# Kernel tuning notes

Measured on AMD Instinct MI355X. Metric: run time of the kernel, lower is better.

The kernel has to match this reference:

```python
import jax, jax.numpy as jnp
import numpy as np

H = 256
L = 5
B = 1024
NL, EL = 65536, 262144
NP_, EP = 131072, 524288
BN_EPS = 1e-5


def _bn_relu(x, gamma, beta):
    # BatchNorm1d (training mode, biased variance) followed by ReLU
    m = x.mean(axis=0)
    v = ((x - m) ** 2).mean(axis=0)
    return jax.nn.relu((x - m) * jax.lax.rsqrt(v + BN_EPS) * gamma + beta)


def _gin_conv(h, src, dst, W1, b1, W2, b2):
    # GINConv, eps=0: mlp(x + sum_{j->i} x_j)
    agg = jax.ops.segment_sum(h[src], dst, num_segments=h.shape[0])
    z = h + agg
    return jax.nn.relu(z @ W1 + b1) @ W2 + b2


def _forward(lig_x, prot_x, lig_embed_W, lig_embed_b, prot_embed_W, prot_embed_b,
             lig_virtual0, prot_virtual0,
             lig_conv_W1, lig_conv_b1, lig_conv_W2, lig_conv_b2,
             lig_vmlp_W, lig_vmlp_b, lig_vmlp_gamma, lig_vmlp_beta,
             prot_conv_W1, prot_conv_b1, prot_conv_W2, prot_conv_b2,
             prot_vmlp_W, prot_vmlp_b, prot_vmlp_gamma, prot_vmlp_beta,
             pred_W1, pred_b1, pred_W2, pred_b2,
             lig_batch, prot_batch, lig_edge_index, prot_edge_index):
    lig_h = lig_x @ lig_embed_W + lig_embed_b        # [NL, H]
    prot_h = prot_x @ prot_embed_W + prot_embed_b    # [NP, H]
    lig_v = jnp.broadcast_to(lig_virtual0, (B, H))
    prot_v = jnp.broadcast_to(prot_virtual0, (B, H))
    l_src, l_dst = lig_edge_index[0], lig_edge_index[1]
    p_src, p_dst = prot_edge_index[0], prot_edge_index[1]
    for i in range(L):
        # ligand branch: virtual-node pool -> MLP -> broadcast, then GIN conv (residual)
        lig_v = lig_v + jax.ops.segment_sum(lig_h, lig_batch, num_segments=B)
        lig_v = _bn_relu(lig_v @ lig_vmlp_W[i] + lig_vmlp_b[i], lig_vmlp_gamma[i], lig_vmlp_beta[i])
        lig_h = lig_h + lig_v[lig_batch]
        lig_h = lig_h + _gin_conv(lig_h, l_src, l_dst, lig_conv_W1[i], lig_conv_b1[i], lig_conv_W2[i], lig_conv_b2[i])
        # protein branch
        prot_v = prot_v + jax.ops.segment_sum(prot_h, prot_batch, num_segments=B)
        prot_v = _bn_relu(prot_v @ prot_vmlp_W[i] + prot_vmlp_b[i], prot_vmlp_gamma[i], prot_vmlp_beta[i])
        prot_h = prot_h + prot_v[prot_batch]
        prot_h = prot_h + _gin_conv(prot_h, p_src, p_dst, prot_conv_W1[i], prot_conv_b1[i], prot_conv_W2[i], prot_conv_b2[i])
    lig_cnt = jax.ops.segment_sum(jnp.ones((lig_h.shape[0],), lig_h.dtype), lig_batch, num_segments=B)
    prot_cnt = jax.ops.segment_sum(jnp.ones((prot_h.shape[0],), prot_h.dtype), prot_batch, num_segments=B)
    lig_pool = jax.ops.segment_sum(lig_h, lig_batch, num_segments=B) / lig_cnt[:, None]
    prot_pool = jax.ops.segment_sum(prot_h, prot_batch, num_segments=B) / prot_cnt[:, None]
    combined = jnp.concatenate([lig_pool, prot_pool], axis=-1)  # [B, 2H]
    return jax.nn.relu(combined @ pred_W1 + pred_b1) @ pred_W2 + pred_b2  # [B, 1]


def setup_inputs() -> dict:
    key = jax.random.key(0)
    ks = jax.random.split(key, 40)
    s = 0.05
    inp = {
        'lig_x': jax.random.normal(ks[0], (NL, 26), jnp.float32),
        'prot_x': jax.random.normal(ks[1], (NP_, 20), jnp.float32),
        'lig_embed_W': jax.random.normal(ks[2], (26, H), jnp.float32) * s,
        'lig_embed_b': jnp.zeros((H,), jnp.float32),
        'prot_embed_W': jax.random.normal(ks[3], (20, H), jnp.float32) * s,
        'prot_embed_b': jnp.zeros((H,), jnp.float32),
        'lig_virtual0': jax.random.normal(ks[4], (1, H), jnp.float32),
        'prot_virtual0': jax.random.normal(ks[5], (1, H), jnp.float32),
        'lig_conv_W1': jax.random.normal(ks[6], (L, H, H), jnp.float32) * s,
        'lig_conv_b1': jnp.zeros((L, H), jnp.float32),
        'lig_conv_W2': jax.random.normal(ks[7], (L, H, H), jnp.float32) * s,
        'lig_conv_b2': jnp.zeros((L, H), jnp.float32),
        'lig_vmlp_W': jax.random.normal(ks[8], (L, H, H), jnp.float32) * s,
        'lig_vmlp_b': jnp.zeros((L, H), jnp.float32),
        'lig_vmlp_gamma': jnp.ones((L, H), jnp.float32),
        'lig_vmlp_beta': jnp.zeros((L, H), jnp.float32),
        'prot_conv_W1': jax.random.normal(ks[9], (L, H, H), jnp.float32) * s,
        'prot_conv_b1': jnp.zeros((L, H), jnp.float32),
        'prot_conv_W2': jax.random.normal(ks[10], (L, H, H), jnp.float32) * s,
        'prot_conv_b2': jnp.zeros((L, H), jnp.float32),
        'prot_vmlp_W': jax.random.normal(ks[11], (L, H, H), jnp.float32) * s,
        'prot_vmlp_b': jnp.zeros((L, H), jnp.float32),
        'prot_vmlp_gamma': jnp.ones((L, H), jnp.float32),
        'prot_vmlp_beta': jnp.zeros((L, H), jnp.float32),
        'pred_W1': jax.random.normal(ks[12], (2 * H, H), jnp.float32) * s,
        'pred_b1': jnp.zeros((H,), jnp.float32),
        'pred_W2': jax.random.normal(ks[13], (H, 1), jnp.float32) * s,
        'pred_b2': jnp.zeros((1,), jnp.float32),
        # sorted batch ids covering all B graphs (PyG-style contiguous batching)
        'lig_batch': (jnp.arange(NL, dtype=jnp.int32) * B) // NL,
        'prot_batch': (jnp.arange(NP_, dtype=jnp.int32) * B) // NP_,
        'lig_edge_index': jax.random.randint(ks[14], (2, EL), 0, NL, jnp.int32),
        'prot_edge_index': jax.random.randint(ks[15], (2, EP), 0, NP_, jnp.int32),
    }
    return inp


def reference(lig_x, prot_x, lig_embed_W, lig_embed_b, prot_embed_W, prot_embed_b,
              lig_virtual0, prot_virtual0,
              lig_conv_W1, lig_conv_b1, lig_conv_W2, lig_conv_b2,
              lig_vmlp_W, lig_vmlp_b, lig_vmlp_gamma, lig_vmlp_beta,
              prot_conv_W1, prot_conv_b1, prot_conv_W2, prot_conv_b2,
              prot_vmlp_W, prot_vmlp_b, prot_vmlp_gamma, prot_vmlp_beta,
              pred_W1, pred_b1, pred_W2, pred_b2,
              lig_batch, prot_batch, lig_edge_index, prot_edge_index):
    return _forward(lig_x, prot_x, lig_embed_W, lig_embed_b, prot_embed_W, prot_embed_b,
                    lig_virtual0, prot_virtual0,
                    lig_conv_W1, lig_conv_b1, lig_conv_W2, lig_conv_b2,
                    lig_vmlp_W, lig_vmlp_b, lig_vmlp_gamma, lig_vmlp_beta,
                    prot_conv_W1, prot_conv_b1, prot_conv_W2, prot_conv_b2,
                    prot_vmlp_W, prot_vmlp_b, prot_vmlp_gamma, prot_vmlp_beta,
                    pred_W1, pred_b1, pred_W2, pred_b2,
                    lig_batch, prot_batch, lig_edge_index, prot_edge_index)
```

## Files before the change

kernel.cpp:

```cpp
#include <hip/hip_runtime.h>

#define H_DIM 256
#define NLAYER 5
#define BGRAPH 1024
#define CAP 24

typedef __attribute__((ext_vector_type(8))) short short8;
typedef __attribute__((ext_vector_type(4))) float f32x4;
typedef const __attribute__((address_space(1))) unsigned int* gas_ptr;
typedef __attribute__((address_space(3))) unsigned int* las_ptr;

struct __align__(8) us4 { unsigned short x, y, z, w; };

__device__ __forceinline__ float b2f(unsigned short u) {
    union { float f; unsigned v; } c; c.v = ((unsigned)u) << 16; return c.f;
}
__device__ __forceinline__ unsigned short f2b(float f) {
    union { float f; unsigned v; } c; c.f = f;
    return (unsigned short)((c.v + 0x7fffu + ((c.v >> 16) & 1u)) >> 16);
}

__global__ __launch_bounds__(256) void embed_kernel(
    const float* __restrict__ x, const float* __restrict__ W,
    const float* __restrict__ b, unsigned short* __restrict__ h, int K)
{
    __shared__ float xs[256];
    const int m0 = blockIdx.x * 8;
    const int tid = threadIdx.x;
    if (tid < 8 * K) xs[tid] = x[(size_t)m0 * K + tid];
    __syncthreads();
    const int n = tid;
    float acc[8] = {0.f,0.f,0.f,0.f,0.f,0.f,0.f,0.f};
    for (int k = 0; k < K; ++k) {
        const float w = W[k * H_DIM + n];
        #pragma unroll
        for (int r = 0; r < 8; ++r) acc[r] += xs[r * K + k] * w;
    }
    const float bb = b[n];
    #pragma unroll
    for (int r = 0; r < 8; ++r)
        h[(size_t)(m0 + r) * H_DIM + n] = f2b(acc[r] + bb);
}

__global__ __launch_bounds__(256) void init_v_kernel(
    const float* __restrict__ lig0, const float* __restrict__ prot0,
    float* __restrict__ lig_v, float* __restrict__ prot_v)
{
    const int b = blockIdx.x, n = threadIdx.x;
    lig_v[b * H_DIM + n]  = lig0[n];
    prot_v[b * H_DIM + n] = prot0[n];
}

__global__ __launch_bounds__(256) void wprep_kernel(
    const float* __restrict__ W, unsigned short* __restrict__ Wt)
{
    __shared__ float t[64][65];
    const int l = blockIdx.z;
    const int k0 = blockIdx.x * 64, n0 = blockIdx.y * 64;
    const int tid = threadIdx.x;
    const int c = tid & 63, r4 = tid >> 6;
    const float* Wl = W + (size_t)l * 65536;
    unsigned short* Wtl = Wt + (size_t)l * 65536;
    #pragma unroll
    for (int i = 0; i < 16; ++i) {
        const int r = i * 4 + r4;
        t[r][c] = Wl[(size_t)(k0 + r) * 256 + n0 + c];
    }
    __syncthreads();
    #pragma unroll
    for (int i = 0; i < 16; ++i) {
        const int nn = i * 4 + r4;
        const int n = n0 + nn;
        const int x = (n >> 1) & 3;
        const int s = ((c >> 3) & 3) ^ x;
        const int kaddr = k0 + (c & ~31) + (s << 3) + (c & 7);
        Wtl[(size_t)n * 256 + kaddr] = f2b(t[c][nn]);
    }
}

__global__ __launch_bounds__(256) void bucket_build_kernel(
    const int* __restrict__ src, const int* __restrict__ dst, int E,
    int* __restrict__ deg, int* __restrict__ bucket)
{
    const int e = blockIdx.x * 256 + threadIdx.x;
    if (e >= E) return;
    const int d = dst[e], s = src[e];
    const int slot = atomicAdd(&deg[d], 1);
    if (slot < CAP) bucket[(size_t)d * CAP + slot] = s;
}

__global__ __launch_bounds__(256) void pool_add_kernel(
    const unsigned short* __restrict__ h, float* __restrict__ v, int cnt)
{
    const int b = blockIdx.x, n = threadIdx.x;
    const unsigned short* hp = &h[(size_t)b * cnt * H_DIM + n];
    float s = 0.f;
    #pragma unroll 8
    for (int r = 0; r < cnt; ++r) s += b2f(hp[(size_t)r * H_DIM]);
    v[b * H_DIM + n] += s;
}

__global__ __launch_bounds__(256) void v_add_kernel(
    float* __restrict__ v, const float* __restrict__ hsum)
{
    const int idx = blockIdx.x * 256 + threadIdx.x;
    v[idx] += hsum[idx];
}

template<bool RELU>
__global__ __launch_bounds__(256) void gemm_small_kernel(
    const float* __restrict__ A, const float* __restrict__ W,
    const float* __restrict__ bias, float* __restrict__ C,
    int M, int N, int K)
{
    constexpr int BM = 32, BN = 64, BK = 32, TM = 2;
    __shared__ __align__(16) float As[BK][BM + 4];
    __shared__ __align__(16) float Bs[BK][BN];
    const int tid = threadIdx.x;
    const int tx = tid & 15;
    const int ty = tid >> 4;
    const int m0 = blockIdx.x * BM;
    const int n0 = blockIdx.y * BN;

    float acc[TM][4] = {};

    for (int kt = 0; kt < K; kt += BK) {
        {
            const int row = tid >> 3, kq = tid & 7;
            const float4 a = *(const float4*)&A[(size_t)(m0 + row) * K + kt + kq * 4];
            As[kq * 4 + 0][row] = a.x;
            As[kq * 4 + 1][row] = a.y;
            As[kq * 4 + 2][row] = a.z;
            As[kq * 4 + 3][row] = a.w;
        }
        #pragma unroll
        for (int i = 0; i < 2; ++i) {
            const int f = tid + i * 256;
            const int row = f >> 4, c4 = f & 15;
            *(float4*)&Bs[row][c4 * 4] =
                *(const float4*)&W[(size_t)(kt + row) * N + n0 + c4 * 4];
        }
        __syncthreads();
        #pragma unroll
        for (int kk = 0; kk < BK; ++kk) {
            const float4 bv = *(const float4*)&Bs[kk][tx * 4];
            #pragma unroll
            for (int im = 0; im < TM; ++im) {
                const float a = As[kk][ty * TM + im];
                acc[im][0] += a * bv.x; acc[im][1] += a * bv.y;
                acc[im][2] += a * bv.z; acc[im][3] += a * bv.w;
            }
        }
        __syncthreads();
    }

    const float4 bb = *(const float4*)&bias[n0 + tx * 4];
    #pragma unroll
    for (int im = 0; im < TM; ++im) {
        const int m = m0 + ty * TM + im;
        float4 r;
        r.x = acc[im][0] + bb.x; r.y = acc[im][1] + bb.y;
        r.z = acc[im][2] + bb.z; r.w = acc[im][3] + bb.w;
        if constexpr (RELU) {
            r.x = fmaxf(r.x, 0.f); r.y = fmaxf(r.y, 0.f);
            r.z = fmaxf(r.z, 0.f); r.w = fmaxf(r.w, 0.f);
        }
        *(float4*)&C[(size_t)m * N + n0 + tx * 4] = r;
    }
}

__global__ __launch_bounds__(512) void conv_fused2_kernel(
    const unsigned short* __restrict__ Hin,
    const int* __restrict__ deg, const int* __restrict__ bucket,
    const int* __restrict__ batch, const float* __restrict__ v,
    const unsigned short* __restrict__ Wt1, const float* __restrict__ b1,
    const unsigned short* __restrict__ Wt2, const float* __restrict__ b2,
    unsigned short* __restrict__ Hout, float* __restrict__ hsum)
{
    constexpr int K = 256, BK = 32;
    __shared__ __align__(16) unsigned short U[64 * 264];
    __shared__ __align__(16) unsigned short Bs[256 * 32];
    const int tid  = threadIdx.x;
    const int lane = tid & 63;
    const int wid  = tid >> 6;
    const int wr   = wid >> 2;
    const int wc   = wid & 3;
    const int q    = lane >> 4;
    const int l15  = lane & 15;
    const int m0   = blockIdx.x * 64;
    const int albase = (tid & ~63) * 16;
    const int bq0  = batch[m0];
    const float* __restrict__ vg = v + (size_t)bq0 * H_DIM;

    {
        const float4 vm = *(const float4*)&vg[lane * 4];
        for (int r8 = 0; r8 < 8; ++r8) {
            const int lr = wid * 8 + r8;
            const int m = m0 + lr;
            const us4 hv = *(const us4*)&Hin[(size_t)m * H_DIM + lane * 4];
            float4 acc = { b2f(hv.x) + vm.x, b2f(hv.y) + vm.y,
                           b2f(hv.z) + vm.z, b2f(hv.w) + vm.w };
            int cnt = deg[m]; if (cnt > CAP) cnt = CAP;
            const int* bp = &bucket[(size_t)m * CAP];
            for (int i = 0; i < cnt; i += 4) {
                const int4 s4 = *(const int4*)&bp[i];
                const int rem = cnt - i;
                us4 a0, a1, a2, a3;
                int q0, q1, q2, q3;
                a0 = *(const us4*)&Hin[(size_t)s4.x * H_DIM + lane * 4];
                q0 = batch[s4.x];
                if (rem > 1) { a1 = *(const us4*)&Hin[(size_t)s4.y * H_DIM + lane * 4]; q1 = batch[s4.y]; }
                if (rem > 2) { a2 = *(const us4*)&Hin[(size_t)s4.z * H_DIM + lane * 4]; q2 = batch[s4.z]; }
                if (rem > 3) { a3 = *(const us4*)&Hin[(size_t)s4.w * H_DIM + lane * 4]; q3 = batch[s4.w]; }
                {
                    const float4 w0 = *(const float4*)&v[(size_t)q0 * H_DIM + lane * 4];
                    acc.x += b2f(a0.x) + w0.x; acc.y += b2f(a0.y) + w0.y;
                    acc.z += b2f(a0.z) + w0.z; acc.w += b2f(a0.w) + w0.w;
                }
                if (rem > 1) {
                    const float4 w1 = *(const float4*)&v[(size_t)q1 * H_DIM + lane * 4];
                    acc.x += b2f(a1.x) + w1.x; acc.y += b2f(a1.y) + w1.y;
                    acc.z += b2f(a1.z) + w1.z; acc.w += b2f(a1.w) + w1.w;
                }
                if (rem > 2) {
                    const float4 w2 = *(const float4*)&v[(size_t)q2 * H_DIM + lane * 4];
                    acc.x += b2f(a2.x) + w2.x; acc.y += b2f(a2.y) + w2.y;
                    acc.z += b2f(a2.z) + w2.z; acc.w += b2f(a2.w) + w2.w;
                }
                if (rem > 3) {
                    const float4 w3 = *(const float4*)&v[(size_t)q3 * H_DIM + lane * 4];
                    acc.x += b2f(a3.x) + w3.x; acc.y += b2f(a3.y) + w3.y;
                    acc.z += b2f(a3.z) + w3.z; acc.w += b2f(a3.w) + w3.w;
                }
            }
            us4 o = { f2b(acc.x), f2b(acc.y), f2b(acc.z), f2b(acc.w) };
            const int ab = lr * 512 + ((lane * 8) ^ ((lr & 7) << 4));
            *(us4*)((char*)U + ab) = o;
        }
    }
    __syncthreads();

    f32x4 acc[2][4];
    #pragma unroll
    for (int i = 0; i < 2; ++i)
        #pragma unroll
        for (int j = 0; j < 4; ++j) acc[i][j] = (f32x4){0.f, 0.f, 0.f, 0.f};

    for (int kt = 0; kt < K; kt += BK) {
        #pragma unroll
        for (int i = 0; i < 2; ++i) {
            const int c = tid + i * 512;
            __builtin_amdgcn_global_load_lds(
                (gas_ptr)&Wt1[(size_t)(c >> 2) * K + kt + (c & 3) * 8],
                (las_ptr)((char*)Bs + albase + i * 8192), 16, 0, 0);
        }
        __syncthreads();
        short8 av[2], bv[4];
        #pragma unroll
        for (int mi = 0; mi < 2; ++mi) {
            const int lrow = wr * 32 + mi * 16 + l15;
            const int ab = lrow * 512 + ((kt * 2 + q * 16) ^ ((lrow & 7) << 4));
            av[mi] = *(const short8*)((char*)U + ab);
        }
        #pragma unroll
        for (int ni = 0; ni < 4; ++ni) {
            const int n = wc * 64 + ni * 16 + l15;
            const int bb = n * 64 + ((q * 16) ^ (((n >> 1) & 3) << 4));
            bv[ni] = *(const short8*)((char*)Bs + bb);
        }
        #pragma unroll
        for (int mi = 0; mi < 2; ++mi)
            #pragma unroll
            for (int ni = 0; ni < 4; ++ni)
                acc[mi][ni] = __builtin_amdgcn_mfma_f32_16x16x32_bf16(
                    av[mi], bv[ni], acc[mi][ni], 0, 0, 0);
        __syncthreads();
    }

    #pragma unroll
    for (int ni = 0; ni < 4; ++ni) {
        const int col = wc * 64 + ni * 16 + l15;
        const float bb = b1[col];
        #pragma unroll
        for (int mi = 0; mi < 2; ++mi)
            #pragma unroll
            for (int j = 0; j < 4; ++j) {
                const int row = wr * 32 + mi * 16 + q * 4 + j;
                U[row * 264 + col] = f2b(fmaxf(acc[mi][ni][j] + bb, 0.f));
            }
    }
    #pragma unroll
    for (int i = 0; i < 2; ++i)
        #pragma unroll
        for (int j = 0; j < 4; ++j) acc[i][j] = (f32x4){0.f, 0.f, 0.f, 0.f};
    __syncthreads();

    for (int kt = 0; kt < K; kt += BK) {
        #pragma unroll
        for (int i = 0; i < 2; ++i) {
            const int c = tid + i * 512;
            __builtin_amdgcn_global_load_lds(
                (gas_ptr)&Wt2[(size_t)(c >> 2) * K + kt + (c & 3) * 8],
                (las_ptr)((char*)Bs + albase + i * 8192), 16, 0, 0);
        }
        __syncthreads();
        short8 av[2], bv[4];
        #pragma unroll
        for (int mi = 0; mi < 2; ++mi) {
            const int lrow = wr * 32 + mi * 16 + l15;
            av[mi] = *(const short8*)&U[lrow * 264 + kt + q * 8];
        }
        #pragma unroll
        for (int ni = 0; ni < 4; ++ni) {
            const int n = wc * 64 + ni * 16 + l15;
            const int bb = n * 64 + ((q * 16) ^ (((n >> 1) & 3) << 4));
            bv[ni] = *(const short8*)((char*)Bs + bb);
        }
        #pragma unroll
        for (int mi = 0; mi < 2; ++mi)
            #pragma unroll
            for (int ni = 0; ni < 4; ++ni)
                acc[mi][ni] = __builtin_amdgcn_mfma_f32_16x16x32_bf16(
                    av[mi], bv[ni], acc[mi][ni], 0, 0, 0);
        __syncthreads();
    }

    float* hl = (float*)Bs;
    if (tid < 256) hl[tid] = 0.f;
    __syncthreads();

    int cols[4]; float b2c[4], vc[4];
    #pragma unroll
    for (int ni = 0; ni < 4; ++ni) {
        cols[ni] = wc * 64 + ni * 16 + l15;
        b2c[ni] = b2[cols[ni]];
        vc[ni]  = vg[cols[ni]];
    }
    float lsum[4] = {0.f, 0.f, 0.f, 0.f};
    #pragma unroll
    for (int mi = 0; mi < 2; ++mi)
        #pragma unroll
        for (int j = 0; j < 4; ++j) {
            const int row = m0 + wr * 32 + mi * 16 + q * 4 + j;
            const unsigned short* hip_ = &Hin[(size_t)row * H_DIM];
            unsigned short* hop = &Hout[(size_t)row * H_DIM];
            #pragma unroll
            for (int ni = 0; ni < 4; ++ni) {
                const float val = b2f(hip_[cols[ni]]) + vc[ni]
                                + acc[mi][ni][j] + b2c[ni];
                hop[cols[ni]] = f2b(val);
                lsum[ni] += val;
            }
        }
    #pragma unroll
    for (int ni = 0; ni < 4; ++ni) atomicAdd(&hl[cols[ni]], lsum[ni]);
    __syncthreads();
    if (tid < 256) atomicAdd(&hsum[(size_t)bq0 * H_DIM + tid], hl[tid]);
}

__global__ __launch_bounds__(256) void bn_part_kernel(
    const float* __restrict__ vtmp, float* __restrict__ part)
{
    const int g = blockIdx.x, n = threadIdx.x;
    float s = 0.f, s2 = 0.f;
    #pragma unroll 8
    for (int r = 0; r < 32; ++r) {
        const float x = vtmp[(size_t)(g * 32 + r) * H_DIM + n];
        s += x; s2 += x * x;
    }
    part[g * H_DIM + n] = s;
    part[32 * H_DIM + g * H_DIM + n] = s2;
}

__global__ __launch_bounds__(256) void bn_finalize_kernel(
    const float* __restrict__ part, const float* __restrict__ gamma,
    const float* __restrict__ beta, float* __restrict__ scale,
    float* __restrict__ shift)
{
    const int n = threadIdx.x;
    float s = 0.f, s2 = 0.f;
    #pragma unroll 8
    for (int g = 0; g < 32; ++g) {
        s  += part[g * H_DIM + n];
        s2 += part[32 * H_DIM + g * H_DIM + n];
    }
    const float mean = s * (1.f / BGRAPH);
    const float var  = s2 * (1.f / BGRAPH) - mean * mean;
    const float sc   = gamma[n] * rsqrtf(var + 1e-5f);
    scale[n] = sc;
    shift[n] = beta[n] - mean * sc;
}

__global__ __launch_bounds__(256) void bn_relu_kernel(
    const float* __restrict__ vtmp, const float* __restrict__ scale,
    const float* __restrict__ shift, float* __restrict__ v)
{
    const int idx = blockIdx.x * 256 + threadIdx.x;
    const int n = idx & 255;
    v[idx] = fmaxf(vtmp[idx] * scale[n] + shift[n], 0.f);
}

__global__ __launch_bounds__(256) void pool_hsum_kernel(
    const float* __restrict__ hl, const float* __restrict__ hp,
    float* __restrict__ comb)
{
    const int b = blockIdx.x, n = threadIdx.x;
    comb[(size_t)b * 512 + n]       = hl[(size_t)b * H_DIM + n] * (1.f / 64.f);
    comb[(size_t)b * 512 + 256 + n] = hp[(size_t)b * H_DIM + n] * (1.f / 128.f);
}

__global__ __launch_bounds__(256) void pred_final_kernel(
    const float* __restrict__ hidden, const float* __restrict__ W2,
    const float* __restrict__ b2, float* __restrict__ out)
{
    const int b = blockIdx.x, t = threadIdx.x;
    float p = hidden[(size_t)b * H_DIM + t] * W2[t];
    #pragma unroll
    for (int off = 32; off >= 1; off >>= 1) p += __shfl_down(p, off);
    __shared__ float red[4];
    if ((t & 63) == 0) red[t >> 6] = p;
    __syncthreads();
    if (t == 0) out[b] = red[0] + red[1] + red[2] + red[3] + b2[0];
}

extern "C" void kernel_launch(void* const* d_in, const int* in_sizes, int n_in,
                              void* d_out, int out_size, void* d_ws, size_t ws_size,
                              hipStream_t stream)
{
    const int NL = 65536, NP = 131072, EL = 262144, EP = 524288;
    const int B = BGRAPH, H = H_DIM;

    const float* lig_x        = (const float*)d_in[0];
    const float* prot_x       = (const float*)d_in[1];
    const float* lig_embed_W  = (const float*)d_in[2];
    const float* lig_embed_b  = (const float*)d_in[3];
    const float* prot_embed_W = (const float*)d_in[4];
    const float* prot_embed_b = (const float*)d_in[5];
    const float* lig_virtual0 = (const float*)d_in[6];
    const float* prot_virtual0= (const float*)d_in[7];
    const float* lig_conv_W1  = (const float*)d_in[8];
    const float* lig_conv_b1  = (const float*)d_in[9];
    const float* lig_conv_W2  = (const float*)d_in[10];
    const float* lig_conv_b2  = (const float*)d_in[11];
    const float* lig_vmlp_W   = (const float*)d_in[12];
    const float* lig_vmlp_b   = (const float*)d_in[13];
    const float* lig_vmlp_g   = (const float*)d_in[14];
    const float* lig_vmlp_be  = (const float*)d_in[15];
    const float* prot_conv_W1 = (const float*)d_in[16];
    const float* prot_conv_b1 = (const float*)d_in[17];
    const float* prot_conv_W2 = (const float*)d_in[18];
    const float* prot_conv_b2 = (const float*)d_in[19];
    const float* prot_vmlp_W  = (const float*)d_in[20];
    const float* prot_vmlp_b  = (const float*)d_in[21];
    const float* prot_vmlp_g  = (const float*)d_in[22];
    const float* prot_vmlp_be = (const float*)d_in[23];
    const float* pred_W1      = (const float*)d_in[24];
    const float* pred_b1      = (const float*)d_in[25];
    const float* pred_W2      = (const float*)d_in[26];
    const float* pred_b2      = (const float*)d_in[27];
    const int* lig_batch      = (const int*)d_in[28];
    const int* prot_batch     = (const int*)d_in[29];
    const int* lig_ei         = (const int*)d_in[30];
    const int* prot_ei        = (const int*)d_in[31];

    float* ws = (float*)d_ws;
    float* lig_v    = ws;
    float* prot_v   = lig_v    + (size_t)B * H;
    float* vtmp     = prot_v   + (size_t)B * H;
    float* scale    = vtmp     + (size_t)B * H;
    float* shift    = scale    + H;
    float* part     = shift    + H;
    float* comb     = part     + 64 * H;
    float* hidden   = comb     + (size_t)B * 2 * H;
    float* hsum_lig = hidden   + (size_t)B * H;
    float* hsum_prot= hsum_lig + (size_t)B * H;
    unsigned short* lig_h0  = (unsigned short*)(hsum_prot + (size_t)B * H);
    unsigned short* lig_h1  = lig_h0  + (size_t)NL * H;
    unsigned short* prot_h0 = lig_h1  + (size_t)NL * H;
    unsigned short* prot_h1 = prot_h0 + (size_t)NP * H;
    unsigned short* wt_lw1  = prot_h1 + (size_t)NP * H;
    unsigned short* wt_lw2  = wt_lw1 + (size_t)NLAYER * H * H;
    unsigned short* wt_pw1  = wt_lw2 + (size_t)NLAYER * H * H;
    unsigned short* wt_pw2  = wt_pw1 + (size_t)NLAYER * H * H;
    int* deg_lig  = (int*)(wt_pw2 + (size_t)NLAYER * H * H);
    int* deg_prot = deg_lig  + NL;
    int* bkt_lig  = deg_prot + NP;
    int* bkt_prot = bkt_lig  + (size_t)NL * CAP;

    hipMemsetAsync(deg_lig, 0, (size_t)(NL + NP) * sizeof(int), stream);
    bucket_build_kernel<<<EL / 256, 256, 0, stream>>>(
        lig_ei, lig_ei + EL, EL, deg_lig, bkt_lig);
    bucket_build_kernel<<<EP / 256, 256, 0, stream>>>(
        prot_ei, prot_ei + EP, EP, deg_prot, bkt_prot);
    wprep_kernel<<<dim3(4, 4, NLAYER), 256, 0, stream>>>(lig_conv_W1, wt_lw1);
    wprep_kernel<<<dim3(4, 4, NLAYER), 256, 0, stream>>>(lig_conv_W2, wt_lw2);
    wprep_kernel<<<dim3(4, 4, NLAYER), 256, 0, stream>>>(prot_conv_W1, wt_pw1);
    wprep_kernel<<<dim3(4, 4, NLAYER), 256, 0, stream>>>(prot_conv_W2, wt_pw2);

    embed_kernel<<<NL / 8, 256, 0, stream>>>(lig_x, lig_embed_W, lig_embed_b, lig_h0, 26);
    embed_kernel<<<NP / 8, 256, 0, stream>>>(prot_x, prot_embed_W, prot_embed_b, prot_h0, 20);
    init_v_kernel<<<B, 256, 0, stream>>>(lig_virtual0, prot_virtual0, lig_v, prot_v);

    auto layer = [&](int i, unsigned short* h_in, unsigned short* h_out,
                     int Nn, int cnt, float* v, float* hsum,
                     const float* vW, const float* vb, const float* vg, const float* vbe,
                     const unsigned short* Wt1, const float* b1,
                     const unsigned short* Wt2, const float* b2,
                     const int* batch, const int* deg, const int* bkt) {
        if (i == 0)
            pool_add_kernel<<<B, 256, 0, stream>>>(h_in, v, cnt);
        else
            v_add_kernel<<<B, 256, 0, stream>>>(v, hsum);
        gemm_small_kernel<false><<<dim3(B / 32, 4), 256, 0, stream>>>(
            v, vW, vb, vtmp, B, H, H);
        bn_part_kernel<<<32, 256, 0, stream>>>(vtmp, part);
        bn_finalize_kernel<<<1, 256, 0, stream>>>(part, vg, vbe, scale, shift);
        bn_relu_kernel<<<B, 256, 0, stream>>>(vtmp, scale, shift, v);
        hipMemsetAsync(hsum, 0, (size_t)B * H * sizeof(float), stream);
        conv_fused2_kernel<<<Nn / 64, 512, 0, stream>>>(
            h_in, deg, bkt, batch, v, Wt1, b1, Wt2, b2, h_out, hsum);
    };

    for (int i = 0; i < NLAYER; ++i) {
        const size_t wo = (size_t)i * H * H;
        const size_t bo = (size_t)i * H;
        unsigned short* lin  = (i & 1) ? lig_h1  : lig_h0;
        unsigned short* lout = (i & 1) ? lig_h0  : lig_h1;
        unsigned short* pin  = (i & 1) ? prot_h1 : prot_h0;
        unsigned short* pout = (i & 1) ? prot_h0 : prot_h1;
        layer(i, lin, lout, NL, 64, lig_v, hsum_lig,
              lig_vmlp_W + wo, lig_vmlp_b + bo, lig_vmlp_g + bo, lig_vmlp_be + bo,
              wt_lw1 + wo, lig_conv_b1 + bo, wt_lw2 + wo, lig_conv_b2 + bo,
              lig_batch, deg_lig, bkt_lig);
        layer(i, pin, pout, NP, 128, prot_v, hsum_prot,
              prot_vmlp_W + wo, prot_vmlp_b + bo, prot_vmlp_g + bo, prot_vmlp_be + bo,
              wt_pw1 + wo, prot_conv_b1 + bo, wt_pw2 + wo, prot_conv_b2 + bo,
              prot_batch, deg_prot, bkt_prot);
    }

    pool_hsum_kernel<<<B, 256, 0, stream>>>(hsum_lig, hsum_prot, comb);
    gemm_small_kernel<true><<<dim3(B / 32, 4), 256, 0, stream>>>(
        comb, pred_W1, pred_b1, hidden, B, H, 2 * H);
    pred_final_kernel<<<B, 256, 0, stream>>>(hidden, pred_W2, pred_b2, (float*)d_out);
}
```

Before: 1.849 ms.

## Batch lig/prot virtual-node MLP, fuse BN stats, and load MFMA weights pre-fragmented

Merges the ligand and protein virtual-node MLP steps into single launches. The GEMM folds in the hsum add and accumulates the BatchNorm sum and sum-of-squares with atomics, and a single apply kernel then normalises both branches. This replaces the v_add, bn_part, bn_finalize and bn_relu launches. The conv kernel now reads weights straight from global memory in a pre-shuffled MFMA fragment layout instead of staging them through LDS with a barrier per k-step, so it needs less shared memory. The risks are more global weight traffic per block, which relies on cache hits, and variance computed from atomically accumulated E[x^2]-mean^2.

```diff
diff --git a/kernel.cpp b/kernel.cpp
--- a/kernel.cpp
+++ b/kernel.cpp
@@ -7,8 +7,6 @@
 
 typedef __attribute__((ext_vector_type(8))) short short8;
 typedef __attribute__((ext_vector_type(4))) float f32x4;
-typedef const __attribute__((address_space(1))) unsigned int* gas_ptr;
-typedef __attribute__((address_space(3))) unsigned int* las_ptr;
 
 struct __align__(8) us4 { unsigned short x, y, z, w; };
 
@@ -51,31 +49,27 @@
     prot_v[b * H_DIM + n] = prot0[n];
 }
 
-__global__ __launch_bounds__(256) void wprep_kernel(
-    const float* __restrict__ W, unsigned short* __restrict__ Wt)
-{
-    __shared__ float t[64][65];
-    const int l = blockIdx.z;
-    const int k0 = blockIdx.x * 64, n0 = blockIdx.y * 64;
-    const int tid = threadIdx.x;
-    const int c = tid & 63, r4 = tid >> 6;
+__global__ __launch_bounds__(64) void wprep_kernel(
+    const float* __restrict__ W, unsigned short* __restrict__ Wf)
+{
+    const int kb = blockIdx.x, nb = blockIdx.y, l = blockIdx.z;
+    const int lane = threadIdx.x, q = lane >> 4, l15 = lane & 15;
     const float* Wl = W + (size_t)l * 65536;
-    unsigned short* Wtl = Wt + (size_t)l * 65536;
-    #pragma unroll
-    for (int i = 0; i < 16; ++i) {
-        const int r = i * 4 + r4;
-        t[r][c] = Wl[(size_t)(k0 + r) * 256 + n0 + c];
-    }
-    __syncthreads();
-    #pragma unroll
-    for (int i = 0; i < 16; ++i) {
-        const int nn = i * 4 + r4;
-        const int n = n0 + nn;
-        const int x = (n >> 1) & 3;
-        const int s = ((c >> 3) & 3) ^ x;
-        const int kaddr = k0 + (c & ~31) + (s << 3) + (c & 7);
-        Wtl[(size_t)n * 256 + kaddr] = f2b(t[c][nn]);
-    }
+    unsigned short* dst = Wf + (size_t)l * 65536
+                        + ((size_t)(kb * 16 + nb) * 64 + lane) * 8;
+    const int kbase = kb * 32 + q * 8;
+    const int n = nb * 16 + l15;
+    us4 o0, o1;
+    o0.x = f2b(Wl[(size_t)(kbase + 0) * 256 + n]);
+    o0.y = f2b(Wl[(size_t)(kbase + 1) * 256 + n]);
+    o0.z = f2b(Wl[(size_t)(kbase + 2) * 256 + n]);
+    o0.w = f2b(Wl[(size_t)(kbase + 3) * 256 + n]);
+    o1.x = f2b(Wl[(size_t)(kbase + 4) * 256 + n]);
+    o1.y = f2b(Wl[(size_t)(kbase + 5) * 256 + n]);
+    o1.z = f2b(Wl[(size_t)(kbase + 6) * 256 + n]);
+    o1.w = f2b(Wl[(size_t)(kbase + 7) * 256 + n]);
+    *(us4*)dst = o0;
+    *(us4*)(dst + 4) = o1;
 }
 
 __global__ __launch_bounds__(256) void bucket_build_kernel(
@@ -89,33 +83,40 @@
     if (slot < CAP) bucket[(size_t)d * CAP + slot] = s;
 }
 
-__global__ __launch_bounds__(256) void pool_add_kernel(
-    const unsigned short* __restrict__ h, float* __restrict__ v, int cnt)
-{
-    const int b = blockIdx.x, n = threadIdx.x;
+__global__ __launch_bounds__(256) void pool0_kernel(
+    const unsigned short* __restrict__ hL, const unsigned short* __restrict__ hP,
+    float* __restrict__ hsL, float* __restrict__ hsP)
+{
+    const int br = blockIdx.y, b = blockIdx.x, n = threadIdx.x;
+    const unsigned short* h = br ? hP : hL;
+    float* hs = br ? hsP : hsL;
+    const int cnt = br ? 128 : 64;
     const unsigned short* hp = &h[(size_t)b * cnt * H_DIM + n];
     float s = 0.f;
     #pragma unroll 8
     for (int r = 0; r < cnt; ++r) s += b2f(hp[(size_t)r * H_DIM]);
-    v[b * H_DIM + n] += s;
-}
-
-__global__ __launch_bounds__(256) void v_add_kernel(
-    float* __restrict__ v, const float* __restrict__ hsum)
-{
-    const int idx = blockIdx.x * 256 + threadIdx.x;
-    v[idx] += hsum[idx];
-}
-
-template<bool RELU>
-__global__ __launch_bounds__(256) void gemm_small_kernel(
-    const float* __restrict__ A, const float* __restrict__ W,
-    const float* __restrict__ bias, float* __restrict__ C,
-    int M, int N, int K)
-{
-    constexpr int BM = 32, BN = 64, BK = 32, TM = 2;
+    hs[(size_t)b * H_DIM + n] = s;
+}
+
+__global__ __launch_bounds__(256) void vmlp_gemm_kernel(
+    const float* __restrict__ vL, const float* __restrict__ hsL,
+    const float* __restrict__ WL, const float* __restrict__ bL,
+    const float* __restrict__ vP, const float* __restrict__ hsP,
+    const float* __restrict__ WP, const float* __restrict__ bP,
+    float* __restrict__ vtL, float* __restrict__ vtP,
+    float* __restrict__ part)
+{
+    constexpr int BM = 32, BN = 64, BK = 32, TM = 2, K = H_DIM, N = H_DIM;
     __shared__ __align__(16) float As[BK][BM + 4];
     __shared__ __align__(16) float Bs[BK][BN];
+    __shared__ float st[2][64];
+    const int br = blockIdx.z;
+    const float* v    = br ? vP  : vL;
+    const float* hsum = br ? hsP : hsL;
+    const float* W    = br ? WP  : WL;
+    const float* bias = br ? bP  : bL;
+    float* vt = br ? vtP : vtL;
+    float* pt = part + br * 512;
     const int tid = threadIdx.x;
     const int tx = tid & 15;
     const int ty = tid >> 4;
@@ -127,7 +128,10 @@
     for (int kt = 0; kt < K; kt += BK) {
         {
             const int row = tid >> 3, kq = tid & 7;
-            const float4 a = *(const float4*)&A[(size_t)(m0 + row) * K + kt + kq * 4];
+            const size_t ao = (size_t)(m0 + row) * K + kt + kq * 4;
+            float4 a = *(const float4*)&v[ao];
+            const float4 h4 = *(const float4*)&hsum[ao];
+            a.x += h4.x; a.y += h4.y; a.z += h4.z; a.w += h4.w;
             As[kq * 4 + 0][row] = a.x;
             As[kq * 4 + 1][row] = a.y;
             As[kq * 4 + 2][row] = a.z;
@@ -154,32 +158,72 @@
         __syncthreads();
     }
 
+    if (tid < 128) ((float*)st)[tid] = 0.f;
+    __syncthreads();
+
     const float4 bb = *(const float4*)&bias[n0 + tx * 4];
+    float cs[4] = {0.f,0.f,0.f,0.f}, cq[4] = {0.f,0.f,0.f,0.f};
     #pragma unroll
     for (int im = 0; im < TM; ++im) {
         const int m = m0 + ty * TM + im;
         float4 r;
         r.x = acc[im][0] + bb.x; r.y = acc[im][1] + bb.y;
         r.z = acc[im][2] + bb.z; r.w = acc[im][3] + bb.w;
-        if constexpr (RELU) {
-            r.x = fmaxf(r.x, 0.f); r.y = fmaxf(r.y, 0.f);
-            r.z = fmaxf(r.z, 0.f); r.w = fmaxf(r.w, 0.f);
-        }
-        *(float4*)&C[(size_t)m * N + n0 + tx * 4] = r;
-    }
-}
-
-__global__ __launch_bounds__(512) void conv_fused2_kernel(
+        *(float4*)&vt[(size_t)m * N + n0 + tx * 4] = r;
+        cs[0] += r.x; cq[0] += r.x * r.x;
+        cs[1] += r.y; cq[1] += r.y * r.y;
+        cs[2] += r.z; cq[2] += r.z * r.z;
+        cs[3] += r.w; cq[3] += r.w * r.w;
+    }
+    #pragma unroll
+    for (int c = 0; c < 4; ++c) {
+        atomicAdd(&st[0][tx * 4 + c], cs[c]);
+        atomicAdd(&st[1][tx * 4 + c], cq[c]);
+    }
+    __syncthreads();
+    if (tid < 64) {
+        atomicAdd(&pt[n0 + tid], st[0][tid]);
+        atomicAdd(&pt[256 + n0 + tid], st[1][tid]);
+    }
+}
+
+__global__ __launch_bounds__(256) void vmlp_apply_kernel(
+    const float* __restrict__ part,
+    const float* __restrict__ gL, const float* __restrict__ beL,
+    const float* __restrict__ gP, const float* __restrict__ beP,
+    const float* __restrict__ vtL, const float* __restrict__ vtP,
+    float* __restrict__ vL, float* __restrict__ vP)
+{
+    const int br = blockIdx.y, n = threadIdx.x;
+    const float* pt = part + br * 512;
+    const float* g  = br ? gP  : gL;
+    const float* be = br ? beP : beL;
+    const float* vt = br ? vtP : vtL;
+    float* v = br ? vP : vL;
+    const float s  = pt[n];
+    const float s2 = pt[256 + n];
+    const float mean = s * (1.f / BGRAPH);
+    const float var  = s2 * (1.f / BGRAPH) - mean * mean;
+    const float sc = g[n] * rsqrtf(var + 1e-5f);
+    const float sh = be[n] - mean * sc;
+    #pragma unroll
+    for (int r = 0; r < 4; ++r) {
+        const size_t i = (size_t)(blockIdx.x * 4 + r) * H_DIM + n;
+        v[i] = fmaxf(vt[i] * sc + sh, 0.f);
+    }
+}
+
+__global__ __launch_bounds__(512) void conv_fused3_kernel(
     const unsigned short* __restrict__ Hin,
     const int* __restrict__ deg, const int* __restrict__ bucket,
     const int* __restrict__ batch, const float* __restrict__ v,
-    const unsigned short* __restrict__ Wt1, const float* __restrict__ b1,
-    const unsigned short* __restrict__ Wt2, const float* __restrict__ b2,
+    const unsigned short* __restrict__ Wf1, const float* __restrict__ b1,
+    const unsigned short* __restrict__ Wf2, const float* __restrict__ b2,
     unsigned short* __restrict__ Hout, float* __restrict__ hsum)
 {
-    constexpr int K = 256, BK = 32;
-    __shared__ __align__(16) unsigned short U[64 * 264];
-    __shared__ __align__(16) unsigned short Bs[256 * 32];
+    __shared__ __align__(16) unsigned short U[64 * 256];
+    __shared__ float hl[256];
+    char* Ub = (char*)U;
     const int tid  = threadIdx.x;
     const int lane = tid & 63;
     const int wid  = tid >> 6;
@@ -188,9 +232,10 @@
     const int q    = lane >> 4;
     const int l15  = lane & 15;
     const int m0   = blockIdx.x * 64;
-    const int albase = (tid & ~63) * 16;
     const int bq0  = batch[m0];
     const float* __restrict__ vg = v + (size_t)bq0 * H_DIM;
+
+    if (tid < 256) hl[tid] = 0.f;
 
     {
         const float4 vm = *(const float4*)&vg[lane * 4];
@@ -235,7 +280,7 @@
             }
             us4 o = { f2b(acc.x), f2b(acc.y), f2b(acc.z), f2b(acc.w) };
             const int ab = lr * 512 + ((lane * 8) ^ ((lr & 7) << 4));
-            *(us4*)((char*)U + ab) = o;
+            *(us4*)(Ub + ab) = o;
         }
     }
     __syncthreads();
@@ -246,36 +291,26 @@
         #pragma unroll
         for (int j = 0; j < 4; ++j) acc[i][j] = (f32x4){0.f, 0.f, 0.f, 0.f};
 
-    for (int kt = 0; kt < K; kt += BK) {
-        #pragma unroll
-        for (int i = 0; i < 2; ++i) {
-            const int c = tid + i * 512;
-            __builtin_amdgcn_global_load_lds(
-                (gas_ptr)&Wt1[(size_t)(c >> 2) * K + kt + (c & 3) * 8],
-                (las_ptr)((char*)Bs + albase + i * 8192), 16, 0, 0);
-        }
-        __syncthreads();
-        short8 av[2], bv[4];
-        #pragma unroll
-        for (int mi = 0; mi < 2; ++mi) {
-            const int lrow = wr * 32 + mi * 16 + l15;
-            const int ab = lrow * 512 + ((kt * 2 + q * 16) ^ ((lrow & 7) << 4));
-            av[mi] = *(const short8*)((char*)U + ab);
-        }
+    const int arow = wr * 32 + l15;
+    const int rowb0 = arow * 512;
+    const int rowb1 = rowb0 + 16 * 512;
+    const int xorv = (l15 & 7) << 4;
+    const unsigned short* wb1 = Wf1 + ((size_t)(wc * 4) * 64 + lane) * 8;
+    const unsigned short* wb2 = Wf2 + ((size_t)(wc * 4) * 64 + lane) * 8;
+
+    #pragma unroll 2
+    for (int kb = 0; kb < 8; ++kb) {
+        const int c0 = (kb * 64 + q * 16) ^ xorv;
+        const short8 av0 = *(const short8*)(Ub + rowb0 + c0);
+        const short8 av1 = *(const short8*)(Ub + rowb1 + c0);
         #pragma unroll
         for (int ni = 0; ni < 4; ++ni) {
-            const int n = wc * 64 + ni * 16 + l15;
-            const int bb = n * 64 + ((q * 16) ^ (((n >> 1) & 3) << 4));
-            bv[ni] = *(const short8*)((char*)Bs + bb);
-        }
-        #pragma unroll
-        for (int mi = 0; mi < 2; ++mi)
-            #pragma unroll
-            for (int ni = 0; ni < 4; ++ni)
-                acc[mi][ni] = __builtin_amdgcn_mfma_f32_16x16x32_bf16(
-                    av[mi], bv[ni], acc[mi][ni], 0, 0, 0);
-        __syncthreads();
-    }
+            const short8 bv = *(const short8*)&wb1[(size_t)kb * 8192 + ni * 512];
+            acc[0][ni] = __builtin_amdgcn_mfma_f32_16x16x32_bf16(av0, bv, acc[0][ni], 0, 0, 0);
+            acc[1][ni] = __builtin_amdgcn_mfma_f32_16x16x32_bf16(av1, bv, acc[1][ni], 0, 0, 0);
+        }
+    }
+    __syncthreads();
 
     #pragma unroll
     for (int ni = 0; ni < 4; ++ni) {
@@ -286,7 +321,8 @@
             #pragma unroll
             for (int j = 0; j < 4; ++j) {
                 const int row = wr * 32 + mi * 16 + q * 4 + j;
-                U[row * 264 + col] = f2b(fmaxf(acc[mi][ni][j] + bb, 0.f));
+                const int tb = row * 512 + ((col * 2) ^ ((row & 7) << 4));
+                *(unsigned short*)(Ub + tb) = f2b(fmaxf(acc[mi][ni][j] + bb, 0.f));
             }
     }
     #pragma unroll
@@ -295,39 +331,18 @@
         for (int j = 0; j < 4; ++j) acc[i][j] = (f32x4){0.f, 0.f, 0.f, 0.f};
     __syncthreads();
 
-    for (int kt = 0; kt < K; kt += BK) {
-        #pragma unroll
-        for (int i = 0; i < 2; ++i) {
-            const int c = tid + i * 512;
-            __builtin_amdgcn_global_load_lds(
-                (gas_ptr)&Wt2[(size_t)(c >> 2) * K + kt + (c & 3) * 8],
-                (las_ptr)((char*)Bs + albase + i * 8192), 16, 0, 0);
-        }
-        __syncthreads();
-        short8 av[2], bv[4];
-        #pragma unroll
-        for (int mi = 0; mi < 2; ++mi) {
-            const int lrow = wr * 32 + mi * 16 + l15;
-            av[mi] = *(const short8*)&U[lrow * 264 + kt + q * 8];
-        }
+    #pragma unroll 2
+    for (int kb = 0; kb < 8; ++kb) {
+        const int c0 = (kb * 64 + q * 16) ^ xorv;
+        const short8 av0 = *(const short8*)(Ub + rowb0 + c0);
+        const short8 av1 = *(const short8*)(Ub + rowb1 + c0);
         #pragma unroll
         for (int ni = 0; ni < 4; ++ni) {
-            const int n = wc * 64 + ni * 16 + l15;
-            const int bb = n * 64 + ((q * 16) ^ (((n >> 1) & 3) << 4));
-            bv[ni] = *(const short8*)((char*)Bs + bb);
-        }
-        #pragma unroll
-        for (int mi = 0; mi < 2; ++mi)
-            #pragma unroll
-            for (int ni = 0; ni < 4; ++ni)
-                acc[mi][ni] = __builtin_amdgcn_mfma_f32_16x16x32_bf16(
-                    av[mi], bv[ni], acc[mi][ni], 0, 0, 0);
-        __syncthreads();
-    }
-
-    float* hl = (float*)Bs;
-    if (tid < 256) hl[tid] = 0.f;
-    __syncthreads();
+            const short8 bv = *(const short8*)&wb2[(size_t)kb * 8192 + ni * 512];
+            acc[0][ni] = __builtin_amdgcn_mfma_f32_16x16x32_bf16(av0, bv, acc[0][ni], 0, 0, 0);
+            acc[1][ni] = __builtin_amdgcn_mfma_f32_16x16x32_bf16(av1, bv, acc[1][ni], 0, 0, 0);
+        }
+    }
 
     int cols[4]; float b2c[4], vc[4];
     #pragma unroll
@@ -358,46 +373,66 @@
     if (tid < 256) atomicAdd(&hsum[(size_t)bq0 * H_DIM + tid], hl[tid]);
 }
 
-__global__ __launch_bounds__(256) void bn_part_kernel(
-    const float* __restrict__ vtmp, float* __restrict__ part)
-{
-    const int g = blockIdx.x, n = threadIdx.x;
-    float s = 0.f, s2 = 0.f;
-    #pragma unroll 8
-    for (int r = 0; r < 32; ++r) {
-        const float x = vtmp[(size_t)(g * 32 + r) * H_DIM + n];
-        s += x; s2 += x * x;
-    }
-    part[g * H_DIM + n] = s;
-    part[32 * H_DIM + g * H_DIM + n] = s2;
-}
-
-__global__ __launch_bounds__(256) void bn_finalize_kernel(
-    const float* __restrict__ part, const float* __restrict__ gamma,
-    const float* __restrict__ beta, float* __restrict__ scale,
-    float* __restrict__ shift)
-{
-    const int n = threadIdx.x;
-    float s = 0.f, s2 = 0.f;
-    #pragma unroll 8
-    for (int g = 0; g < 32; ++g) {
-        s  += part[g * H_DIM + n];
-        s2 += part[32 * H_DIM + g * H_DIM + n];
-    }
-    const float mean = s * (1.f / BGRAPH);
-    const float var  = s2 * (1.f / BGRAPH) - mean * mean;
-    const float sc   = gamma[n] * rsqrtf(var + 1e-5f);
-    scale[n] = sc;
-    shift[n] = beta[n] - mean * sc;
-}
-
-__global__ __launch_bounds__(256) void bn_relu_kernel(
-    const float* __restrict__ vtmp, const float* __restrict__ scale,
-    const float* __restrict__ shift, float* __restrict__ v)
-{
-    const int idx = blockIdx.x * 256 + threadIdx.x;
-    const int n = idx & 255;
-    v[idx] = fmaxf(vtmp[idx] * scale[n] + shift[n], 0.f);
+template<bool RELU>
+__global__ __launch_bounds__(256) void gemm_small_kernel(
+    const float* __restrict__ A, const float* __restrict__ W,
+    const float* __restrict__ bias, float* __restrict__ C,
+    int M, int N, int K)
+{
+    constexpr int BM = 32, BN = 64, BK = 32, TM = 2;
+    __shared__ __align__(16) float As[BK][BM + 4];
+    __shared__ __align__(16) float Bs[BK][BN];
+    const int tid = threadIdx.x;
+    const int tx = tid & 15;
+    const int ty = tid >> 4;
+    const int m0 = blockIdx.x * BM;
+    const int n0 = blockIdx.y * BN;
+
+    float acc[TM][4] = {};
+
+    for (int kt = 0; kt < K; kt += BK) {
+        {
+            const int row = tid >> 3, kq = tid & 7;
+            const float4 a = *(const float4*)&A[(size_t)(m0 + row) * K + kt + kq * 4];
+            As[kq * 4 + 0][row] = a.x;
+            As[kq * 4 + 1][row] = a.y;
+            As[kq * 4 + 2][row] = a.z;
+            As[kq * 4 + 3][row] = a.w;
+        }
+        #pragma unroll
+        for (int i = 0; i < 2; ++i) {
+            const int f = tid + i * 256;
+            const int row = f >> 4, c4 = f & 15;
+            *(float4*)&Bs[row][c4 * 4] =
+                *(const float4*)&W[(size_t)(kt + row) * N + n0 + c4 * 4];
+        }
+        __syncthreads();
+        #pragma unroll
+        for (int kk = 0; kk < BK; ++kk) {
+            const float4 bv = *(const float4*)&Bs[kk][tx * 4];
+            #pragma unroll
+            for (int im = 0; im < TM; ++im) {
+                const float a = As[kk][ty * TM + im];
+                acc[im][0] += a * bv.x; acc[im][1] += a * bv.y;
+                acc[im][2] += a * bv.z; acc[im][3] += a * bv.w;
+            }
+        }
+        __syncthreads();
+    }
+
+    const float4 bb = *(const float4*)&bias[n0 + tx * 4];
+    #pragma unroll
+    for (int im = 0; im < TM; ++im) {
+        const int m = m0 + ty * TM + im;
+        float4 r;
+        r.x = acc[im][0] + bb.x; r.y = acc[im][1] + bb.y;
+        r.z = acc[im][2] + bb.z; r.w = acc[im][3] + bb.w;
+        if constexpr (RELU) {
+            r.x = fmaxf(r.x, 0.f); r.y = fmaxf(r.y, 0.f);
+            r.z = fmaxf(r.z, 0.f); r.w = fmaxf(r.w, 0.f);
+        }
+        *(float4*)&C[(size_t)m * N + n0 + tx * 4] = r;
+    }
 }
 
 __global__ __launch_bounds__(256) void pool_hsum_kernel(
@@ -466,11 +501,10 @@
     float* ws = (float*)d_ws;
     float* lig_v    = ws;
     float* prot_v   = lig_v    + (size_t)B * H;
-    float* vtmp     = prot_v   + (size_t)B * H;
-    float* scale    = vtmp     + (size_t)B * H;
-    float* shift    = scale    + H;
-    float* part     = shift    + H;
-    float* comb     = part     + 64 * H;
+    float* vtmpL    = prot_v   + (size_t)B * H;
+    float* vtmpP    = vtmpL    + (size_t)B * H;
+    float* part     = vtmpP    + (size_t)B * H;
+    float* comb     = part     + 1024;
     float* hidden   = comb     + (size_t)B * 2 * H;
     float* hsum_lig = hidden   + (size_t)B * H;
     float* hsum_prot= hsum_lig + (size_t)B * H;
@@ -478,11 +512,11 @@
     unsigned short* lig_h1  = lig_h0  + (size_t)NL * H;
     unsigned short* prot_h0 = lig_h1  + (size_t)NL * H;
     unsigned short* prot_h1 = prot_h0 + (size_t)NP * H;
-    unsigned short* wt_lw1  = prot_h1 + (size_t)NP * H;
-    unsigned short* wt_lw2  = wt_lw1 + (size_t)NLAYER * H * H;
-    unsigned short* wt_pw1  = wt_lw2 + (size_t)NLAYER * H * H;
-    unsigned short* wt_pw2  = wt_pw1 + (size_t)NLAYER * H * H;
-    int* deg_lig  = (int*)(wt_pw2 + (size_t)NLAYER * H * H);
+    unsigned short* wf_lw1  = prot_h1 + (size_t)NP * H;
+    unsigned short* wf_lw2  = wf_lw1 + (size_t)NLAYER * H * H;
+    unsigned short* wf_pw1  = wf_lw2 + (size_t)NLAYER * H * H;
+    unsigned short* wf_pw2  = wf_pw1 + (size_t)NLAYER * H * H;
+    int* deg_lig  = (int*)(wf_pw2 + (size_t)NLAYER * H * H);
     int* deg_prot = deg_lig  + NL;
     int* bkt_lig  = deg_prot + NP;
     int* bkt_prot = bkt_lig  + (size_t)NL * CAP;
@@ -492,34 +526,15 @@
         lig_ei, lig_ei + EL, EL, deg_lig, bkt_lig);
     bucket_build_kernel<<<EP / 256, 256, 0, stream>>>(
         prot_ei, prot_ei + EP, EP, deg_prot, bkt_prot);
-    wprep_kernel<<<dim3(4, 4, NLAYER), 256, 0, stream>>>(lig_conv_W1, wt_lw1);
-    wprep_kernel<<<dim3(4, 4, NLAYER), 256, 0, stream>>>(lig_conv_W2, wt_lw2);
-    wprep_kernel<<<dim3(4, 4, NLAYER), 256, 0, stream>>>(prot_conv_W1, wt_pw1);
-    wprep_kernel<<<dim3(4, 4, NLAYER), 256, 0, stream>>>(prot_conv_W2, wt_pw2);
+    wprep_kernel<<<dim3(8, 16, NLAYER), 64, 0, stream>>>(lig_conv_W1, wf_lw1);
+    wprep_kernel<<<dim3(8, 16, NLAYER), 64, 0, stream>>>(lig_conv_W2, wf_lw2);
+    wprep_kernel<<<dim3(8, 16, NLAYER), 64, 0, stream>>>(prot_conv_W1, wf_pw1);
+    wprep_kernel<<<dim3(8, 16, NLAYER), 64, 0, stream>>>(prot_conv_W2, wf_pw2);
 
     embed_kernel<<<NL / 8, 256, 0, stream>>>(lig_x, lig_embed_W, lig_embed_b, lig_h0, 26);
     embed_kernel<<<NP / 8, 256, 0, stream>>>(prot_x, prot_embed_W, prot_embed_b, prot_h0, 20);
     init_v_kernel<<<B, 256, 0, stream>>>(lig_virtual0, prot_virtual0, lig_v, prot_v);
-
-    auto layer = [&](int i, unsigned short* h_in, unsigned short* h_out,
-                     int Nn, int cnt, float* v, float* hsum,
-                     const float* vW, const float* vb, const float* vg, const float* vbe,
-                     const unsigned short* Wt1, const float* b1,
-                     const unsigned short* Wt2, const float* b2,
-                     const int* batch, const int* deg, const int* bkt) {
-        if (i == 0)
-            pool_add_kernel<<<B, 256, 0, stream>>>(h_in, v, cnt);
-        else
-            v_add_kernel<<<B, 256, 0, stream>>>(v, hsum);
-        gemm_small_kernel<false><<<dim3(B / 32, 4), 256, 0, stream>>>(
-            v, vW, vb, vtmp, B, H, H);
-        bn_part_kernel<<<32, 256, 0, stream>>>(vtmp, part);
-        bn_finalize_kernel<<<1, 256, 0, stream>>>(part, vg, vbe, scale, shift);
-        bn_relu_kernel<<<B, 256, 0, stream>>>(vtmp, scale, shift, v);
-        hipMemsetAsync(hsum, 0, (size_t)B * H * sizeof(float), stream);
-        conv_fused2_kernel<<<Nn / 64, 512, 0, stream>>>(
-            h_in, deg, bkt, batch, v, Wt1, b1, Wt2, b2, h_out, hsum);
-    };
+    pool0_kernel<<<dim3(B, 2), 256, 0, stream>>>(lig_h0, prot_h0, hsum_lig, hsum_prot);
 
     for (int i = 0; i < NLAYER; ++i) {
         const size_t wo = (size_t)i * H * H;
@@ -528,14 +543,25 @@
         unsigned short* lout = (i & 1) ? lig_h0  : lig_h1;
         unsigned short* pin  = (i & 1) ? prot_h1 : prot_h0;
         unsigned short* pout = (i & 1) ? prot_h0 : prot_h1;
-        layer(i, lin, lout, NL, 64, lig_v, hsum_lig,
-              lig_vmlp_W + wo, lig_vmlp_b + bo, lig_vmlp_g + bo, lig_vmlp_be + bo,
-              wt_lw1 + wo, lig_conv_b1 + bo, wt_lw2 + wo, lig_conv_b2 + bo,
-              lig_batch, deg_lig, bkt_lig);
-        layer(i, pin, pout, NP, 128, prot_v, hsum_prot,
-              prot_vmlp_W + wo, prot_vmlp_b + bo, prot_vmlp_g + bo, prot_vmlp_be + bo,
-              wt_pw1 + wo, prot_conv_b1 + bo, wt_pw2 + wo, prot_conv_b2 + bo,
-              prot_batch, deg_prot, bkt_prot);
+
+        hipMemsetAsync(part, 0, 1024 * sizeof(float), stream);
+        vmlp_gemm_kernel<<<dim3(32, 4, 2), 256, 0, stream>>>(
+            lig_v, hsum_lig, lig_vmlp_W + wo, lig_vmlp_b + bo,
+            prot_v, hsum_prot, prot_vmlp_W + wo, prot_vmlp_b + bo,
+            vtmpL, vtmpP, part);
+        vmlp_apply_kernel<<<dim3(256, 2), 256, 0, stream>>>(
+            part, lig_vmlp_g + bo, lig_vmlp_be + bo,
+            prot_vmlp_g + bo, prot_vmlp_be + bo,
+            vtmpL, vtmpP, lig_v, prot_v);
+        hipMemsetAsync(hsum_lig, 0, (size_t)2 * B * H * sizeof(float), stream);
+        conv_fused3_kernel<<<NL / 64, 512, 0, stream>>>(
+            lin, deg_lig, bkt_lig, lig_batch, lig_v,
+            wf_lw1 + wo, lig_conv_b1 + bo, wf_lw2 + wo, lig_conv_b2 + bo,
+            lout, hsum_lig);
+        conv_fused3_kernel<<<NP / 64, 512, 0, stream>>>(
+            pin, deg_prot, bkt_prot, prot_batch, prot_v,
+            wf_pw1 + wo, prot_conv_b1 + bo, wf_pw2 + wo, prot_conv_b2 + bo,
+            pout, hsum_prot);
     }
 
     pool_hsum_kernel<<<B, 256, 0, stream>>>(hsum_lig, hsum_prot, comb);
```

After: 1.823 ms. About the same (-1.4%).
